# Kernel optimization log

Measured on AMD Instinct MI355X. Metric: run time of the kernel, lower is better.

The kernel has to match this reference:

```python
import jax, jax.numpy as jnp
import numpy as np

B, S, H, E = 2, 2048, 1024, 16


def setup_inputs() -> dict:
    key = jax.random.key(0)
    k0, k1, k2, k3 = jax.random.split(key, 4)
    tokens = jax.random.normal(k0, (B, S, H), dtype=jnp.float32)
    gate_w = jax.random.normal(k1, (E, H), dtype=jnp.float32) * (H ** -0.5)
    expert_w = jax.random.normal(k2, (E, H, H), dtype=jnp.float32) * (H ** -0.5)
    expert_b = jax.random.normal(k3, (E, H), dtype=jnp.float32) * 0.01
    return {"tokens": tokens, "gate_w": gate_w, "expert_w": expert_w, "expert_b": expert_b}


def reference(tokens, gate_w, expert_w, expert_b):
    b, s, h = tokens.shape
    # gate: Linear(H, E, bias=False) -> logits, softmax, top-2
    logits = jnp.einsum('bsh,eh->bse', tokens, gate_w)
    weights = jax.nn.softmax(logits, axis=-1)
    top2_w, top2_idx = jax.lax.top_k(weights, 2)           # [b,s,2]
    flat = tokens.reshape(b * s, h)                         # [N,H]
    flat_w = top2_w.reshape(b * s, 2)
    flat_idx = top2_idx.reshape(b * s, 2)
    # dense per-expert Linear+ReLU for all tokens (grouped GEMM form)
    y = jax.nn.relu(jnp.einsum('nh,edh->ned', flat, expert_w) + expert_b[None, :, :])  # [N,E,H]
    # gather the two selected experts per token and combine with gate weights
    sel = jnp.take_along_axis(y, flat_idx[:, :, None], axis=1)  # [N,2,H]
    out = jnp.sum(sel * flat_w[:, :, None], axis=1)             # [N,H]
    return out.reshape(b, s, h)
```

## Files before the change

### kernel.cpp

```cpp
#include <hip/hip_runtime.h>
#include <hip/hip_bf16.h>

#define TOKENS 4096
#define HDIM 1024
#define NEXP 16
#define BM 128
#define BN 128
#define BK 64
#define MAX_TILES (TOKENS * 2 / BM + NEXP)

typedef __bf16 bf16x8 __attribute__((ext_vector_type(8)));
typedef float f32x4 __attribute__((ext_vector_type(4)));

__device__ inline void gload16(const void* g, const void* l) {
  __builtin_amdgcn_global_load_lds((const __attribute__((address_space(1))) void*)g,
                                   (__attribute__((address_space(3))) void*)l, 16, 0, 0);
}

__global__ __launch_bounds__(256) void cvt_kernel(const float* __restrict__ src,
                                                  __bf16* __restrict__ dst) {
  int i = blockIdx.x * 256 + threadIdx.x;
  float4 a = ((const float4*)src)[i * 2];
  float4 b = ((const float4*)src)[i * 2 + 1];
  bf16x8 v;
  v[0] = (__bf16)a.x; v[1] = (__bf16)a.y; v[2] = (__bf16)a.z; v[3] = (__bf16)a.w;
  v[4] = (__bf16)b.x; v[5] = (__bf16)b.y; v[6] = (__bf16)b.z; v[7] = (__bf16)b.w;
  ((bf16x8*)dst)[i] = v;
}

__global__ __launch_bounds__(256) void gate_kernel(
    const float* __restrict__ tokens, const float* __restrict__ gate_w,
    int* __restrict__ tok_idx, float* __restrict__ tok_w) {
  int lane = threadIdx.x & 63;
  int wv = threadIdx.x >> 6;
  int token = blockIdx.x * 4 + wv;
  const float* trow = tokens + (size_t)token * HDIM;

  float4 tv[4];
#pragma unroll
  for (int s = 0; s < 4; ++s) tv[s] = *(const float4*)(trow + s * 256 + lane * 4);

  float lg[NEXP];
#pragma unroll
  for (int e = 0; e < NEXP; ++e) {
    float d = 0.f;
#pragma unroll
    for (int s = 0; s < 4; ++s) {
      float4 g = *(const float4*)(gate_w + e * HDIM + s * 256 + lane * 4);
      d += tv[s].x * g.x + tv[s].y * g.y + tv[s].z * g.z + tv[s].w * g.w;
    }
#pragma unroll
    for (int off = 32; off; off >>= 1) d += __shfl_xor(d, off);
    lg[e] = d;
  }

  int i0 = 0; float b0 = lg[0];
#pragma unroll
  for (int e = 1; e < NEXP; ++e) if (lg[e] > b0) { b0 = lg[e]; i0 = e; }
  int i1 = -1; float b1 = -1e30f;
#pragma unroll
  for (int e = 0; e < NEXP; ++e) {
    if (e == i0) continue;
    if (lg[e] > b1) { b1 = lg[e]; i1 = e; }
  }
  float s = 0.f;
#pragma unroll
  for (int e = 0; e < NEXP; ++e) s += expf(lg[e] - b0);
  float w0 = 1.0f / s;
  float w1 = expf(b1 - b0) / s;

  if (lane == 0) {
    tok_idx[token * 2 + 0] = i0;
    tok_idx[token * 2 + 1] = i1;
    tok_w[token * 2 + 0] = w0;
    tok_w[token * 2 + 1] = w1;
  }
}

__global__ __launch_bounds__(256) void build_lists_kernel(
    const int* __restrict__ tok_idx, const float* __restrict__ tok_w,
    int* __restrict__ counts, int* __restrict__ list_tok, float* __restrict__ list_w) {
  int e = blockIdx.x;
  __shared__ int cur;
  if (threadIdx.x == 0) cur = 0;
  __syncthreads();
  for (int s = threadIdx.x; s < TOKENS * 2; s += 256) {
    if (tok_idx[s] == e) {
      int pos = atomicAdd(&cur, 1);
      list_tok[e * TOKENS + pos] = s >> 1;
      list_w[e * TOKENS + pos] = tok_w[s];
    }
  }
  __syncthreads();
  if (threadIdx.x == 0) counts[e] = cur;
}

__global__ void plan_kernel(const int* __restrict__ counts, int* __restrict__ tiles,
                            int* __restrict__ n_tiles) {
  if (threadIdx.x == 0) {
    int n = 0;
    for (int e = 0; e < NEXP; ++e) {
      int t = (counts[e] + BM - 1) / BM;
      for (int m = 0; m < t; ++m) { tiles[n * 2] = e; tiles[n * 2 + 1] = m; ++n; }
    }
    *n_tiles = n;
  }
}

__global__ __launch_bounds__(512, 4) void moe_gemm_kernel(
    const __bf16* __restrict__ tok_bf, const __bf16* __restrict__ w_bf,
    const float* __restrict__ expert_b, const int* __restrict__ counts,
    const int* __restrict__ tiles, const int* __restrict__ n_tiles,
    const int* __restrict__ list_tok, const float* __restrict__ list_w,
    float* __restrict__ out) {
  int bx = blockIdx.x;
  if (bx >= *n_tiles) return;
  int e = tiles[bx * 2];
  int mt = tiles[bx * 2 + 1];
  int cnt = counts[e];
  int nt = blockIdx.y;
  const int lbase = e * TOKENS;

  __shared__ __bf16 lds[2][(BM + BN) * BK];

  int tid = threadIdx.x;
  int lane = tid & 63;
  int wv = tid >> 6;

  const __bf16* aptr[2];
  const __bf16* bptr[2];
  int dstb[2];
#pragma unroll
  for (int i = 0; i < 2; ++i) {
    int c = (wv * 2 + i) * 64 + lane;
    int r = c >> 3, kc = c & 7;
    int gr = mt * BM + r;
    int tok = list_tok[lbase + ((gr < cnt) ? gr : (cnt - 1))];
    aptr[i] = tok_bf + (size_t)tok * HDIM + (kc ^ (r & 7)) * 8;
    int d = nt * BN + r;
    bptr[i] = w_bf + (size_t)e * HDIM * HDIM + (size_t)d * HDIM + (kc ^ (r & 7)) * 8;
    dstb[i] = (wv * 2 + i) * 512;
  }

  int wr = (wv >> 2) * 64;
  int wc = (wv & 3) * 32;
  int lr = lane & 15;
  int lk = lane >> 4;

  int aoffr[2][4], boffr[2][2];
#pragma unroll
  for (int kk = 0; kk < 2; ++kk) {
#pragma unroll
    for (int m = 0; m < 4; ++m) {
      int r = wr + m * 16 + lr;
      aoffr[kk][m] = r * BK + (((kk * 4 + lk) ^ (r & 7)) * 8);
    }
#pragma unroll
    for (int n = 0; n < 2; ++n) {
      int d = wc + n * 16 + lr;
      boffr[kk][n] = BM * BK + d * BK + (((kk * 4 + lk) ^ (d & 7)) * 8);
    }
  }

  f32x4 acc[4][2] = {};

#pragma unroll
  for (int i = 0; i < 2; ++i) gload16(aptr[i], &lds[0][dstb[i]]);
#pragma unroll
  for (int i = 0; i < 2; ++i) gload16(bptr[i], &lds[0][BM * BK + dstb[i]]);
  __syncthreads();

  int buf = 0;
  for (int kb = 0; kb < HDIM / BK; ++kb) {
    if (kb + 1 < HDIM / BK) {
      int nb = buf ^ 1;
      int ko = (kb + 1) * BK;
#pragma unroll
      for (int i = 0; i < 2; ++i) gload16(aptr[i] + ko, &lds[nb][dstb[i]]);
#pragma unroll
      for (int i = 0; i < 2; ++i) gload16(bptr[i] + ko, &lds[nb][BM * BK + dstb[i]]);
    }

    bf16x8 af[2][4], bfr[2][2];
#pragma unroll
    for (int kk = 0; kk < 2; ++kk) {
#pragma unroll
      for (int m = 0; m < 4; ++m) af[kk][m] = *(const bf16x8*)(&lds[buf][aoffr[kk][m]]);
#pragma unroll
      for (int n = 0; n < 2; ++n) bfr[kk][n] = *(const bf16x8*)(&lds[buf][boffr[kk][n]]);
    }
#pragma unroll
    for (int kk = 0; kk < 2; ++kk)
#pragma unroll
      for (int m = 0; m < 4; ++m)
#pragma unroll
        for (int n = 0; n < 2; ++n)
          acc[m][n] = __builtin_amdgcn_mfma_f32_16x16x32_bf16(af[kk][m], bfr[kk][n], acc[m][n], 0, 0, 0);

    __syncthreads();
    buf ^= 1;
  }

#pragma unroll
  for (int m = 0; m < 4; ++m) {
#pragma unroll
    for (int j = 0; j < 4; ++j) {
      int rloc = wr + m * 16 + lk * 4 + j;
      int grow = mt * BM + rloc;
      if (grow < cnt) {
        int tok = list_tok[lbase + grow];
        float gw = list_w[lbase + grow];
        float* orow = out + (size_t)tok * HDIM + nt * BN + wc;
        const float* brow = expert_b + e * HDIM + nt * BN + wc;
#pragma unroll
        for (int n = 0; n < 2; ++n) {
          int dcol = n * 16 + lr;
          float v = acc[m][n][j] + brow[dcol];
          v = fmaxf(v, 0.f) * gw;
          atomicAdd(orow + dcol, v);
        }
      }
    }
  }
}

extern "C" void kernel_launch(void* const* d_in, const int* in_sizes, int n_in,
                              void* d_out, int out_size, void* d_ws, size_t ws_size,
                              hipStream_t stream) {
  const float* tokens = (const float*)d_in[0];
  const float* gate_w = (const float*)d_in[1];
  const float* expert_w = (const float*)d_in[2];
  const float* expert_b = (const float*)d_in[3];
  float* out = (float*)d_out;

  int* counts = (int*)d_ws;
  int* n_tiles = counts + 16;
  int* tiles = n_tiles + 16;
  int* tok_idx = tiles + MAX_TILES * 2;
  float* tok_w = (float*)(tok_idx + TOKENS * 2);
  int* list_tok = (int*)(tok_w + TOKENS * 2);
  float* list_w = (float*)(list_tok + NEXP * TOKENS);
  size_t head = (size_t)(list_w + NEXP * TOKENS) - (size_t)d_ws;
  head = (head + 255) & ~(size_t)255;
  __bf16* w_bf = (__bf16*)((char*)d_ws + head);
  __bf16* tok_bf = w_bf + (size_t)NEXP * HDIM * HDIM;

  hipMemsetAsync(d_out, 0, (size_t)out_size * sizeof(float), stream);

  cvt_kernel<<<NEXP * HDIM * HDIM / 8 / 256, 256, 0, stream>>>(expert_w, w_bf);
  cvt_kernel<<<TOKENS * HDIM / 8 / 256, 256, 0, stream>>>(tokens, tok_bf);
  gate_kernel<<<TOKENS / 4, 256, 0, stream>>>(tokens, gate_w, tok_idx, tok_w);
  build_lists_kernel<<<NEXP, 256, 0, stream>>>(tok_idx, tok_w, counts, list_tok, list_w);
  plan_kernel<<<1, 64, 0, stream>>>(counts, tiles, n_tiles);

  dim3 grid(MAX_TILES, HDIM / BN);
  moe_gemm_kernel<<<grid, 512, 0, stream>>>(tok_bf, w_bf, expert_b, counts, tiles, n_tiles,
                                            list_tok, list_w, out);
}
```

Before: 227.7 us.

## Shrink GEMM N tile, swizzle 1D grid, fuse token bf16 cast into gate

The token fp32-to-bf16 conversion moves into the gate kernel, which already reads each token row, so one launch and one full pass over the tokens go away. The grouped GEMM tile shrinks from 128x128 to 128x64, with a new 4x2 wave layout and a higher launch_bounds occupancy hint. The 2D grid becomes a 1D grid with a bid-based swizzle that groups tiles across N, aiming at better L2 reuse and more blocks to spread across CUs. build_lists now uses 1024 threads per block. The smaller tile reloads the A operand more often and issues more atomics per output element.

After: 200.3 us. 12.0% less time.

```diff
diff --git a/kernel.cpp b/kernel.cpp
--- a/kernel.cpp
+++ b/kernel.cpp
@@ -5,11 +5,13 @@
 #define HDIM 1024
 #define NEXP 16
 #define BM 128
-#define BN 128
+#define BN 64
 #define BK 64
-#define MAX_TILES (TOKENS * 2 / BM + NEXP)
+#define MAXP 80
+#define MAXT (MAXP * 16)
 
 typedef __bf16 bf16x8 __attribute__((ext_vector_type(8)));
+typedef __bf16 bf16x4 __attribute__((ext_vector_type(4)));
 typedef float f32x4 __attribute__((ext_vector_type(4)));
 
 __device__ inline void gload16(const void* g, const void* l) {
@@ -30,7 +32,7 @@
 
 __global__ __launch_bounds__(256) void gate_kernel(
     const float* __restrict__ tokens, const float* __restrict__ gate_w,
-    int* __restrict__ tok_idx, float* __restrict__ tok_w) {
+    int* __restrict__ tok_idx, float* __restrict__ tok_w, __bf16* __restrict__ tok_bf) {
   int lane = threadIdx.x & 63;
   int wv = threadIdx.x >> 6;
   int token = blockIdx.x * 4 + wv;
@@ -40,6 +42,14 @@
 #pragma unroll
   for (int s = 0; s < 4; ++s) tv[s] = *(const float4*)(trow + s * 256 + lane * 4);
 
+#pragma unroll
+  for (int s = 0; s < 4; ++s) {
+    bf16x4 v;
+    v[0] = (__bf16)tv[s].x; v[1] = (__bf16)tv[s].y;
+    v[2] = (__bf16)tv[s].z; v[3] = (__bf16)tv[s].w;
+    *(bf16x4*)(tok_bf + (size_t)token * HDIM + s * 256 + lane * 4) = v;
+  }
+
   float lg[NEXP];
 #pragma unroll
   for (int e = 0; e < NEXP; ++e) {
@@ -66,25 +76,22 @@
   float s = 0.f;
 #pragma unroll
   for (int e = 0; e < NEXP; ++e) s += expf(lg[e] - b0);
-  float w0 = 1.0f / s;
-  float w1 = expf(b1 - b0) / s;
-
   if (lane == 0) {
     tok_idx[token * 2 + 0] = i0;
     tok_idx[token * 2 + 1] = i1;
-    tok_w[token * 2 + 0] = w0;
-    tok_w[token * 2 + 1] = w1;
-  }
-}
-
-__global__ __launch_bounds__(256) void build_lists_kernel(
+    tok_w[token * 2 + 0] = 1.0f / s;
+    tok_w[token * 2 + 1] = expf(b1 - b0) / s;
+  }
+}
+
+__global__ __launch_bounds__(1024) void build_lists_kernel(
     const int* __restrict__ tok_idx, const float* __restrict__ tok_w,
     int* __restrict__ counts, int* __restrict__ list_tok, float* __restrict__ list_w) {
   int e = blockIdx.x;
   __shared__ int cur;
   if (threadIdx.x == 0) cur = 0;
   __syncthreads();
-  for (int s = threadIdx.x; s < TOKENS * 2; s += 256) {
+  for (int s = threadIdx.x; s < TOKENS * 2; s += 1024) {
     if (tok_idx[s] == e) {
       int pos = atomicAdd(&cur, 1);
       list_tok[e * TOKENS + pos] = s >> 1;
@@ -96,29 +103,34 @@
 }
 
 __global__ void plan_kernel(const int* __restrict__ counts, int* __restrict__ tiles,
-                            int* __restrict__ n_tiles) {
+                            int* __restrict__ npg) {
   if (threadIdx.x == 0) {
     int n = 0;
     for (int e = 0; e < NEXP; ++e) {
       int t = (counts[e] + BM - 1) / BM;
       for (int m = 0; m < t; ++m) { tiles[n * 2] = e; tiles[n * 2 + 1] = m; ++n; }
     }
-    *n_tiles = n;
-  }
-}
-
-__global__ __launch_bounds__(512, 4) void moe_gemm_kernel(
+    *npg = n;
+  }
+}
+
+__global__ __launch_bounds__(512, 6) void moe_gemm_kernel(
     const __bf16* __restrict__ tok_bf, const __bf16* __restrict__ w_bf,
     const float* __restrict__ expert_b, const int* __restrict__ counts,
-    const int* __restrict__ tiles, const int* __restrict__ n_tiles,
+    const int* __restrict__ tiles, const int* __restrict__ npg,
     const int* __restrict__ list_tok, const float* __restrict__ list_w,
     float* __restrict__ out) {
-  int bx = blockIdx.x;
-  if (bx >= *n_tiles) return;
-  int e = tiles[bx * 2];
-  int mt = tiles[bx * 2 + 1];
+  int npairs = *npg;
+  int n_tiles = npairs * 16;
+  int bid = blockIdx.x;
+  if (bid >= n_tiles) return;
+  int chunk = n_tiles >> 3;
+  int swz = (bid & 7) * chunk + (bid >> 3);
+  int nt = swz / npairs;
+  int pair = swz - nt * npairs;
+  int e = tiles[pair * 2];
+  int mt = tiles[pair * 2 + 1];
   int cnt = counts[e];
-  int nt = blockIdx.y;
   const int lbase = e * TOKENS;
 
   __shared__ __bf16 lds[2][(BM + BN) * BK];
@@ -128,30 +140,36 @@
   int wv = tid >> 6;
 
   const __bf16* aptr[2];
-  const __bf16* bptr[2];
-  int dstb[2];
+  int adst[2];
 #pragma unroll
   for (int i = 0; i < 2; ++i) {
     int c = (wv * 2 + i) * 64 + lane;
     int r = c >> 3, kc = c & 7;
     int gr = mt * BM + r;
-    int tok = list_tok[lbase + ((gr < cnt) ? gr : (cnt - 1))];
+    int tok = list_tok[lbase + min(gr, cnt - 1)];
     aptr[i] = tok_bf + (size_t)tok * HDIM + (kc ^ (r & 7)) * 8;
+    adst[i] = (wv * 2 + i) * 512;
+  }
+  const __bf16* bptr;
+  int bdst;
+  {
+    int c = wv * 64 + lane;
+    int r = c >> 3, kc = c & 7;
     int d = nt * BN + r;
-    bptr[i] = w_bf + (size_t)e * HDIM * HDIM + (size_t)d * HDIM + (kc ^ (r & 7)) * 8;
-    dstb[i] = (wv * 2 + i) * 512;
-  }
-
-  int wr = (wv >> 2) * 64;
-  int wc = (wv & 3) * 32;
+    bptr = w_bf + ((size_t)e * HDIM + d) * HDIM + (kc ^ (r & 7)) * 8;
+    bdst = BM * BK + wv * 512;
+  }
+
   int lr = lane & 15;
   int lk = lane >> 4;
-
-  int aoffr[2][4], boffr[2][2];
+  int wr = (wv & 3) * 32;
+  int wc = (wv >> 2) * 32;
+
+  int aoffr[2][2], boffr[2][2];
 #pragma unroll
   for (int kk = 0; kk < 2; ++kk) {
 #pragma unroll
-    for (int m = 0; m < 4; ++m) {
+    for (int m = 0; m < 2; ++m) {
       int r = wr + m * 16 + lr;
       aoffr[kk][m] = r * BK + (((kk * 4 + lk) ^ (r & 7)) * 8);
     }
@@ -162,12 +180,11 @@
     }
   }
 
-  f32x4 acc[4][2] = {};
-
-#pragma unroll
-  for (int i = 0; i < 2; ++i) gload16(aptr[i], &lds[0][dstb[i]]);
-#pragma unroll
-  for (int i = 0; i < 2; ++i) gload16(bptr[i], &lds[0][BM * BK + dstb[i]]);
+  f32x4 acc[2][2] = {};
+
+#pragma unroll
+  for (int i = 0; i < 2; ++i) gload16(aptr[i], &lds[0][adst[i]]);
+  gload16(bptr, &lds[0][bdst]);
   __syncthreads();
 
   int buf = 0;
@@ -176,23 +193,22 @@
       int nb = buf ^ 1;
       int ko = (kb + 1) * BK;
 #pragma unroll
-      for (int i = 0; i < 2; ++i) gload16(aptr[i] + ko, &lds[nb][dstb[i]]);
-#pragma unroll
-      for (int i = 0; i < 2; ++i) gload16(bptr[i] + ko, &lds[nb][BM * BK + dstb[i]]);
-    }
-
-    bf16x8 af[2][4], bfr[2][2];
+      for (int i = 0; i < 2; ++i) gload16(aptr[i] + ko, &lds[nb][adst[i]]);
+      gload16(bptr + ko, &lds[nb][bdst]);
+    }
+
+    bf16x8 af[2][2], bfr[2][2];
 #pragma unroll
     for (int kk = 0; kk < 2; ++kk) {
 #pragma unroll
-      for (int m = 0; m < 4; ++m) af[kk][m] = *(const bf16x8*)(&lds[buf][aoffr[kk][m]]);
+      for (int m = 0; m < 2; ++m) af[kk][m] = *(const bf16x8*)(&lds[buf][aoffr[kk][m]]);
 #pragma unroll
       for (int n = 0; n < 2; ++n) bfr[kk][n] = *(const bf16x8*)(&lds[buf][boffr[kk][n]]);
     }
 #pragma unroll
     for (int kk = 0; kk < 2; ++kk)
 #pragma unroll
-      for (int m = 0; m < 4; ++m)
+      for (int m = 0; m < 2; ++m)
 #pragma unroll
         for (int n = 0; n < 2; ++n)
           acc[m][n] = __builtin_amdgcn_mfma_f32_16x16x32_bf16(af[kk][m], bfr[kk][n], acc[m][n], 0, 0, 0);
@@ -202,7 +218,7 @@
   }
 
 #pragma unroll
-  for (int m = 0; m < 4; ++m) {
+  for (int m = 0; m < 2; ++m) {
 #pragma unroll
     for (int j = 0; j < 4; ++j) {
       int rloc = wr + m * 16 + lk * 4 + j;
@@ -214,10 +230,9 @@
         const float* brow = expert_b + e * HDIM + nt * BN + wc;
 #pragma unroll
         for (int n = 0; n < 2; ++n) {
-          int dcol = n * 16 + lr;
-          float v = acc[m][n][j] + brow[dcol];
-          v = fmaxf(v, 0.f) * gw;
-          atomicAdd(orow + dcol, v);
+          int dc = n * 16 + lr;
+          float v = acc[m][n][j] + brow[dc];
+          atomicAdd(orow + dc, fmaxf(v, 0.f) * gw);
         }
       }
     }
@@ -234,9 +249,9 @@
   float* out = (float*)d_out;
 
   int* counts = (int*)d_ws;
-  int* n_tiles = counts + 16;
-  int* tiles = n_tiles + 16;
-  int* tok_idx = tiles + MAX_TILES * 2;
+  int* npg = counts + 16;
+  int* tiles = npg + 16;
+  int* tok_idx = tiles + MAXP * 2;
   float* tok_w = (float*)(tok_idx + TOKENS * 2);
   int* list_tok = (int*)(tok_w + TOKENS * 2);
   float* list_w = (float*)(list_tok + NEXP * TOKENS);
@@ -248,12 +263,10 @@
   hipMemsetAsync(d_out, 0, (size_t)out_size * sizeof(float), stream);
 
   cvt_kernel<<<NEXP * HDIM * HDIM / 8 / 256, 256, 0, stream>>>(expert_w, w_bf);
-  cvt_kernel<<<TOKENS * HDIM / 8 / 256, 256, 0, stream>>>(tokens, tok_bf);
-  gate_kernel<<<TOKENS / 4, 256, 0, stream>>>(tokens, gate_w, tok_idx, tok_w);
-  build_lists_kernel<<<NEXP, 256, 0, stream>>>(tok_idx, tok_w, counts, list_tok, list_w);
-  plan_kernel<<<1, 64, 0, stream>>>(counts, tiles, n_tiles);
-
-  dim3 grid(MAX_TILES, HDIM / BN);
-  moe_gemm_kernel<<<grid, 512, 0, stream>>>(tok_bf, w_bf, expert_b, counts, tiles, n_tiles,
+  gate_kernel<<<TOKENS / 4, 256, 0, stream>>>(tokens, gate_w, tok_idx, tok_w, tok_bf);
+  build_lists_kernel<<<NEXP, 1024, 0, stream>>>(tok_idx, tok_w, counts, list_tok, list_w);
+  plan_kernel<<<1, 64, 0, stream>>>(counts, tiles, npg);
+
+  moe_gemm_kernel<<<MAXT, 512, 0, stream>>>(tok_bf, w_bf, expert_b, counts, tiles, npg,
                                             list_tok, list_w, out);
 }
```
